# Kernel tuning notes

Hardware: AMD Instinct MI355X
Metric: run time of the kernel (lower is better)

The kernel has to match this reference:

```python
import jax, jax.numpy as jnp
import numpy as np
import math

B, T, D, H = 4, 1024, 512, 8
DH = D // H


def setup_inputs() -> dict:
    key = jax.random.key(0)
    ks = jax.random.split(key, 8)
    s = 1.0 / math.sqrt(D)
    return {
        "x": jax.random.normal(ks[0], (B, T, D), jnp.float32),
        "Wq_w": jax.random.normal(ks[1], (D, D), jnp.float32) * s,
        "Wq_b": jnp.zeros((D,), jnp.float32),
        "Wk_w": jax.random.normal(ks[2], (D, D), jnp.float32) * s,
        "Wk_b": jnp.zeros((D,), jnp.float32),
        "Wv_w": jax.random.normal(ks[3], (D, D), jnp.float32) * s,
        "Wv_b": jnp.zeros((D,), jnp.float32),
        "Ws_w": jax.random.normal(ks[4], (D, H), jnp.float32) * s,
        "Ws_b": jnp.zeros((H,), jnp.float32),
        "Wo_w": jax.random.normal(ks[5], (D, D), jnp.float32) * s,
        "Wo_b": jnp.zeros((D,), jnp.float32),
    }


def reference(x, Wq_w, Wq_b, Wk_w, Wk_b, Wv_w, Wv_b, Ws_w, Ws_b, Wo_w, Wo_b):
    b, t, d = x.shape
    # projections (weights stored [in, out]; same math as torch Linear)
    q = (x @ Wq_w + Wq_b).reshape(b, t, H, DH).transpose(0, 2, 1, 3)  # [B,H,T,dh]
    k = (x @ Wk_w + Wk_b).reshape(b, t, H, DH).transpose(0, 2, 1, 3)
    v = (x @ Wv_w + Wv_b).reshape(b, t, H, DH).transpose(0, 2, 1, 3)

    logits = jnp.einsum("bhtd,bhsd->bhts", q, k) / math.sqrt(DH)
    series = jax.nn.softmax(logits, axis=-1)  # [B,H,T,T] (dropout p=0 -> no-op)

    sigma = jax.nn.softplus(x @ Ws_w + Ws_b).transpose(0, 2, 1) + 1e-6  # [B,H,T]

    idx = jnp.arange(t, dtype=jnp.float32)
    dist2 = (idx[None, :] - idx[:, None]) ** 2  # [T,T]
    s2 = sigma[..., None] ** 2 + 1e-6           # [B,H,T,1]
    prior = jnp.exp(-dist2[None, None] / (2.0 * s2))
    prior = prior / (prior.sum(axis=-1, keepdims=True) + 1e-9)

    out = jnp.einsum("bhts,bhsd->bhtd", series, v)
    out = out.transpose(0, 2, 1, 3).reshape(b, t, d)
    out = out @ Wo_w + Wo_b
    return out, series, prior, sigma
```

## Files before the change

### kernel.cpp

```cpp
#include <hip/hip_runtime.h>
#include <math.h>

#define BB 4
#define TT 1024
#define DD 512
#define HH 8
#define DHH 64

typedef short bf8_t __attribute__((ext_vector_type(8)));
typedef float f32x4 __attribute__((ext_vector_type(4)));

__device__ __forceinline__ float softplus_f(float z) {
    return fmaxf(z, 0.f) + log1pf(__expf(-fabsf(z)));
}

__device__ __forceinline__ unsigned short f2bf(float f) {
    union { float f; unsigned int u; } v; v.f = f;
    return (unsigned short)((v.u + 0x7FFFu + ((v.u >> 16) & 1u)) >> 16);
}

__device__ __forceinline__ void bar_lgkm() {
    asm volatile("s_waitcnt lgkmcnt(0)" ::: "memory");
    __builtin_amdgcn_s_barrier();
}

__global__ __launch_bounds__(256) void cast_x_kernel(
    const float* __restrict__ x, unsigned short* __restrict__ xbf)
{
    int i = blockIdx.x * 256 + threadIdx.x;
    float4 a = *(const float4*)&x[(size_t)i * 8];
    float4 b = *(const float4*)&x[(size_t)i * 8 + 4];
    union { unsigned short u[8]; int4 v; } o;
    o.u[0] = f2bf(a.x); o.u[1] = f2bf(a.y); o.u[2] = f2bf(a.z); o.u[3] = f2bf(a.w);
    o.u[4] = f2bf(b.x); o.u[5] = f2bf(b.y); o.u[6] = f2bf(b.z); o.u[7] = f2bf(b.w);
    *(int4*)&xbf[(size_t)i * 8] = o.v;
}

__global__ __launch_bounds__(256) void transpose_w_kernel(
    const float* __restrict__ Wq, const float* __restrict__ Wk,
    const float* __restrict__ Wv, const float* __restrict__ Wo,
    const float* __restrict__ Ws,
    unsigned short* __restrict__ wt, unsigned short* __restrict__ woT)
{
    __shared__ float tile[32][33];
    const int tid = threadIdx.x;
    const int z = blockIdx.z;
    if (z == 4) {
        if (blockIdx.x != 0 || blockIdx.y != 0) return;
        #pragma unroll
        for (int i = 0; i < 16; ++i) {
            int idx = i * 256 + tid;
            int k = idx >> 3, n = idx & 7;
            wt[(size_t)(1536 + n) * 512 + k] = f2bf(Ws[idx]);
        }
        return;
    }
    const float* W = (z == 0) ? Wq : (z == 1) ? Wk : (z == 2) ? Wv : Wo;
    unsigned short* dst = (z < 3) ? (wt + (size_t)z * 512 * 512) : woT;
    const int k0 = blockIdx.x * 32, n0 = blockIdx.y * 32;
    const int ty = tid >> 3, tx = tid & 7;

    float4 v = *(const float4*)&W[(size_t)(k0 + ty) * 512 + n0 + tx * 4];
    tile[ty][tx*4+0] = v.x; tile[ty][tx*4+1] = v.y;
    tile[ty][tx*4+2] = v.z; tile[ty][tx*4+3] = v.w;
    __syncthreads();
    ushort4 o;
    o.x = f2bf(tile[tx*4+0][ty]);
    o.y = f2bf(tile[tx*4+1][ty]);
    o.z = f2bf(tile[tx*4+2][ty]);
    o.w = f2bf(tile[tx*4+3][ty]);
    *(ushort4*)&dst[(size_t)(n0 + ty) * 512 + k0 + tx * 4] = o;
}

__global__ __launch_bounds__(256) void proj_mfma_kernel(
    const unsigned short* __restrict__ xbf,
    const unsigned short* __restrict__ wt,
    const float* __restrict__ bq, const float* __restrict__ bk,
    const float* __restrict__ bv, const float* __restrict__ bs,
    unsigned short* __restrict__ qbf, unsigned short* __restrict__ kbf,
    unsigned short* __restrict__ vbf, float* __restrict__ sigma_out)
{
    __shared__ unsigned short a_s[64][64];
    __shared__ unsigned short b_s[64][64];
    const int tid = threadIdx.x;
    const int w = tid >> 6, l = tid & 63, lr = l & 15, lg = l >> 4;
    const int ct = blockIdx.x;
    const int m0 = blockIdx.y * 64;
    const int n0 = ct * 64;

    f32x4 acc[4];
    #pragma unroll
    for (int nb = 0; nb < 4; ++nb) acc[nb] = (f32x4){0.f, 0.f, 0.f, 0.f};

    for (int k0 = 0; k0 < 512; k0 += 64) {
        __syncthreads();
        #pragma unroll
        for (int rep = 0; rep < 2; ++rep) {
            int idx = rep * 256 + tid;
            int row = idx >> 3, cg = idx & 7;
            *(int4*)&a_s[row][(cg ^ (row & 7)) * 8] =
                *(const int4*)&xbf[(size_t)(m0 + row) * 512 + k0 + cg * 8];
            *(int4*)&b_s[row][(cg ^ (row & 7)) * 8] =
                *(const int4*)&wt[(size_t)(n0 + row) * 512 + k0 + cg * 8];
        }
        __syncthreads();
        #pragma unroll
        for (int ks = 0; ks < 2; ++ks) {
            int arow = w * 16 + lr;
            bf8_t af = *(const bf8_t*)&a_s[arow][((ks*4 + lg) ^ (arow & 7)) * 8];
            #pragma unroll
            for (int nb = 0; nb < 4; ++nb) {
                int brow = nb * 16 + lr;
                bf8_t bf = *(const bf8_t*)&b_s[brow][((ks*4 + lg) ^ (brow & 7)) * 8];
                acc[nb] = __builtin_amdgcn_mfma_f32_16x16x32_bf16(af, bf, acc[nb], 0, 0, 0);
            }
        }
    }

    if (ct < 24) {
        const int seg = ct >> 3;
        const int h = ct & 7;
        const float* bias = (seg == 0) ? bq : (seg == 1) ? bk : bv;
        unsigned short* dst = (seg == 0) ? qbf : (seg == 1) ? kbf : vbf;
        const float sc = (seg == 0) ? 0.125f : 1.f;
        #pragma unroll
        for (int nb = 0; nb < 4; ++nb) {
            float bb = bias[h * 64 + nb * 16 + lr];
            #pragma unroll
            for (int r = 0; r < 4; ++r) {
                int m = m0 + w * 16 + lg * 4 + r;
                int b = m >> 10, t = m & 1023;
                dst[((size_t)((b*HH + h)*TT + t)) * 64 + nb * 16 + lr] =
                    f2bf((acc[nb][r] + bb) * sc);
            }
        }
    } else if (lr < 8) {
        float bb = bs[lr];
        #pragma unroll
        for (int r = 0; r < 4; ++r) {
            int m = m0 + w * 16 + lg * 4 + r;
            int b = m >> 10, t = m & 1023;
            sigma_out[(size_t)(b*HH + lr)*TT + t] = softplus_f(acc[0][r] + bb) + 1e-6f;
        }
    }
}

__global__ __launch_bounds__(256) void attn_kernel(
    const unsigned short* __restrict__ qbf,
    const unsigned short* __restrict__ kbf,
    const unsigned short* __restrict__ vbf,
    const float* __restrict__ sigma,
    float* __restrict__ series, float* __restrict__ prior,
    unsigned short* __restrict__ obf)
{
    __shared__ unsigned short k_lds[2][64][72];
    __shared__ unsigned short v_lds[2][64][64];
    __shared__ unsigned short p_lds[4][16][72];

    const int tid = threadIdx.x;
    const int w  = tid >> 6, l = tid & 63;
    const int lr = l & 15,  lg = l >> 4;
    const int bh = blockIdx.y;
    const int qr = blockIdx.x * 64 + w * 16;

    const int srow = tid >> 3, scg = tid & 7;
    const unsigned short* kb = kbf + (size_t)bh * TT * 64;
    const unsigned short* vb = vbf + (size_t)bh * TT * 64;

    bf8_t aq[2];
    {
        const unsigned short* qrow = &qbf[((size_t)bh * TT + qr + lr) * 64];
        aq[0] = *(const bf8_t*)&qrow[lg * 8];
        aq[1] = *(const bf8_t*)&qrow[32 + lg * 8];
    }

    int4 kreg0, kreg1, vreg0, vreg1;

    float psum[4] = {0.f, 0.f, 0.f, 0.f};
    kreg0 = *(const int4*)&kb[(size_t)srow * 64 + scg * 8];
    kreg1 = *(const int4*)&kb[(size_t)(32 + srow) * 64 + scg * 8];
    *(int4*)&k_lds[0][srow][scg * 8] = kreg0;
    *(int4*)&k_lds[0][32 + srow][scg * 8] = kreg1;
    bar_lgkm();

    for (int st = 0; st < 16; ++st) {
        const int cur = st & 1;
        if (st < 15) {
            kreg0 = *(const int4*)&kb[(size_t)((st+1)*64 + srow) * 64 + scg * 8];
            kreg1 = *(const int4*)&kb[(size_t)((st+1)*64 + 32 + srow) * 64 + scg * 8];
        }
        #pragma unroll
        for (int nb = 0; nb < 4; ++nb) {
            f32x4 acc = {0.f, 0.f, 0.f, 0.f};
            #pragma unroll
            for (int c = 0; c < 2; ++c) {
                bf8_t bk = *(const bf8_t*)&k_lds[cur][nb * 16 + lr][c * 32 + lg * 8];
                acc = __builtin_amdgcn_mfma_f32_16x16x32_bf16(aq[c], bk, acc, 0, 0, 0);
            }
            #pragma unroll
            for (int r = 0; r < 4; ++r) psum[r] += __expf(acc[r]);
        }
        if (st < 15) {
            *(int4*)&k_lds[cur ^ 1][srow][scg * 8] = kreg0;
            *(int4*)&k_lds[cur ^ 1][32 + srow][scg * 8] = kreg1;
            bar_lgkm();
        }
    }
    #pragma unroll
    for (int r = 0; r < 4; ++r) {
        psum[r] += __shfl_xor(psum[r], 1);
        psum[r] += __shfl_xor(psum[r], 2);
        psum[r] += __shfl_xor(psum[r], 4);
        psum[r] += __shfl_xor(psum[r], 8);
    }
    float inv[4];
    #pragma unroll
    for (int r = 0; r < 4; ++r) inv[r] = 1.f / psum[r];

    f32x4 oacc[4];
    #pragma unroll
    for (int nb = 0; nb < 4; ++nb) oacc[nb] = (f32x4){0.f, 0.f, 0.f, 0.f};

    kreg0 = *(const int4*)&kb[(size_t)srow * 64 + scg * 8];
    kreg1 = *(const int4*)&kb[(size_t)(32 + srow) * 64 + scg * 8];
    vreg0 = *(const int4*)&vb[(size_t)srow * 64 + scg * 8];
    vreg1 = *(const int4*)&vb[(size_t)(32 + srow) * 64 + scg * 8];
    *(int4*)&k_lds[0][srow][scg * 8] = kreg0;
    *(int4*)&k_lds[0][32 + srow][scg * 8] = kreg1;
    {
        const unsigned short* pv0 = (const unsigned short*)&vreg0;
        const unsigned short* pv1 = (const unsigned short*)&vreg1;
        #pragma unroll
        for (int j = 0; j < 8; ++j) {
            int row = scg * 8 + j;
            int g0 = ((srow >> 3) ^ j ^ scg) & 7;
            int g1 = ((srow >> 3) ^ 4 ^ j ^ scg) & 7;
            v_lds[0][row][g0 * 8 + (srow & 7)] = pv0[j];
            v_lds[0][row][g1 * 8 + (srow & 7)] = pv1[j];
        }
    }
    bar_lgkm();

    for (int st = 0; st < 16; ++st) {
        const int cur = st & 1;
        if (st < 15) {
            kreg0 = *(const int4*)&kb[(size_t)((st+1)*64 + srow) * 64 + scg * 8];
            kreg1 = *(const int4*)&kb[(size_t)((st+1)*64 + 32 + srow) * 64 + scg * 8];
            vreg0 = *(const int4*)&vb[(size_t)((st+1)*64 + srow) * 64 + scg * 8];
            vreg1 = *(const int4*)&vb[(size_t)((st+1)*64 + 32 + srow) * 64 + scg * 8];
        }

        #pragma unroll
        for (int nb = 0; nb < 4; ++nb) {
            f32x4 acc = {0.f, 0.f, 0.f, 0.f};
            #pragma unroll
            for (int c = 0; c < 2; ++c) {
                bf8_t bk = *(const bf8_t*)&k_lds[cur][nb * 16 + lr][c * 32 + lg * 8];
                acc = __builtin_amdgcn_mfma_f32_16x16x32_bf16(aq[c], bk, acc, 0, 0, 0);
            }
            #pragma unroll
            for (int r = 0; r < 4; ++r) {
                float e = __expf(acc[r]);
                series[((size_t)bh * TT + qr + lg * 4 + r) * TT + st * 64 + nb * 16 + lr]
                    = e * inv[r];
                p_lds[w][lg * 4 + r][nb * 16 + lr] = f2bf(e);
            }
        }

        bf8_t pa0 = *(const bf8_t*)&p_lds[w][lr][lg * 8];
        bf8_t pa1 = *(const bf8_t*)&p_lds[w][lr][32 + lg * 8];
        #pragma unroll
        for (int nb = 0; nb < 4; ++nb) {
            #pragma unroll
            for (int c = 0; c < 2; ++c) {
                int row = nb * 16 + lr;
                int gsw = ((c * 4 + lg) ^ (row & 7) ^ (row >> 3)) & 7;
                bf8_t bv = *(const bf8_t*)&v_lds[cur][row][gsw * 8];
                oacc[nb] = __builtin_amdgcn_mfma_f32_16x16x32_bf16(
                    (c == 0) ? pa0 : pa1, bv, oacc[nb], 0, 0, 0);
            }
        }

        {
            int t = qr + st;
            float sg = sigma[(size_t)bh * TT + t];
            float cc = 1.f / (2.f * (sg * sg + 1e-6f));
            float e[16]; float sum = 0.f;
            #pragma unroll
            for (int j = 0; j < 16; ++j) {
                float d = (float)(t - (j * 64 + l));
                e[j] = __expf(-(d * d) * cc);
                sum += e[j];
            }
            sum += __shfl_xor(sum, 32);
            sum += __shfl_xor(sum, 16);
            sum += __shfl_xor(sum, 8);
            sum += __shfl_xor(sum, 4);
            sum += __shfl_xor(sum, 2);
            sum += __shfl_xor(sum, 1);
            float pinv = 1.f / (sum + 1e-9f);
            float* pr = prior + ((size_t)bh * TT + t) * TT;
            #pragma unroll
            for (int j = 0; j < 16; ++j) pr[j * 64 + l] = e[j] * pinv;
        }

        if (st < 15) {
            *(int4*)&k_lds[cur ^ 1][srow][scg * 8] = kreg0;
            *(int4*)&k_lds[cur ^ 1][32 + srow][scg * 8] = kreg1;
            const unsigned short* pv0 = (const unsigned short*)&vreg0;
            const unsigned short* pv1 = (const unsigned short*)&vreg1;
            #pragma unroll
            for (int j = 0; j < 8; ++j) {
                int row = scg * 8 + j;
                int g0 = ((srow >> 3) ^ j ^ scg) & 7;
                int g1 = ((srow >> 3) ^ 4 ^ j ^ scg) & 7;
                v_lds[cur ^ 1][row][g0 * 8 + (srow & 7)] = pv0[j];
                v_lds[cur ^ 1][row][g1 * 8 + (srow & 7)] = pv1[j];
            }
            bar_lgkm();
        }
    }

    const int b = bh >> 3, h = bh & 7;
    #pragma unroll
    for (int nb = 0; nb < 4; ++nb)
        #pragma unroll
        for (int r = 0; r < 4; ++r) {
            int t = qr + lg * 4 + r;
            obf[((size_t)(b * TT + t)) * 512 + h * 64 + nb * 16 + lr] =
                f2bf(oacc[nb][r] * inv[r]);
        }
}

__global__ __launch_bounds__(256) void outproj_mfma_kernel(
    const unsigned short* __restrict__ obf,
    const unsigned short* __restrict__ woT,
    const float* __restrict__ bo, float* __restrict__ out)
{
    __shared__ unsigned short a_s[64][64];
    __shared__ unsigned short b_s[64][64];
    const int tid = threadIdx.x;
    const int w = tid >> 6, l = tid & 63, lr = l & 15, lg = l >> 4;
    const int n0 = blockIdx.x * 64;
    const int m0 = blockIdx.y * 64;

    f32x4 acc[4];
    #pragma unroll
    for (int nb = 0; nb < 4; ++nb) acc[nb] = (f32x4){0.f, 0.f, 0.f, 0.f};

    for (int k0 = 0; k0 < 512; k0 += 64) {
        __syncthreads();
        #pragma unroll
        for (int rep = 0; rep < 2; ++rep) {
            int idx = rep * 256 + tid;
            int row = idx >> 3, cg = idx & 7;
            *(int4*)&a_s[row][(cg ^ (row & 7)) * 8] =
                *(const int4*)&obf[(size_t)(m0 + row) * 512 + k0 + cg * 8];
            *(int4*)&b_s[row][(cg ^ (row & 7)) * 8] =
                *(const int4*)&woT[(size_t)(n0 + row) * 512 + k0 + cg * 8];
        }
        __syncthreads();
        #pragma unroll
        for (int ks = 0; ks < 2; ++ks) {
            int arow = w * 16 + lr;
            bf8_t af = *(const bf8_t*)&a_s[arow][((ks*4 + lg) ^ (arow & 7)) * 8];
            #pragma unroll
            for (int nb = 0; nb < 4; ++nb) {
                int brow = nb * 16 + lr;
                bf8_t bf = *(const bf8_t*)&b_s[brow][((ks*4 + lg) ^ (brow & 7)) * 8];
                acc[nb] = __builtin_amdgcn_mfma_f32_16x16x32_bf16(af, bf, acc[nb], 0, 0, 0);
            }
        }
    }

    #pragma unroll
    for (int nb = 0; nb < 4; ++nb) {
        float bb = bo[n0 + nb * 16 + lr];
        #pragma unroll
        for (int r = 0; r < 4; ++r) {
            int m = m0 + w * 16 + lg * 4 + r;
            out[(size_t)m * 512 + n0 + nb * 16 + lr] = acc[nb][r] + bb;
        }
    }
}

extern "C" void kernel_launch(void* const* d_in, const int* in_sizes, int n_in,
                              void* d_out, int out_size, void* d_ws, size_t ws_size,
                              hipStream_t stream)
{
    const float* x    = (const float*)d_in[0];
    const float* Wq_w = (const float*)d_in[1];
    const float* Wq_b = (const float*)d_in[2];
    const float* Wk_w = (const float*)d_in[3];
    const float* Wk_b = (const float*)d_in[4];
    const float* Wv_w = (const float*)d_in[5];
    const float* Wv_b = (const float*)d_in[6];
    const float* Ws_w = (const float*)d_in[7];
    const float* Ws_b = (const float*)d_in[8];
    const float* Wo_w = (const float*)d_in[9];
    const float* Wo_b = (const float*)d_in[10];

    float* out    = (float*)d_out;
    float* series = out + (size_t)BB*TT*DD;
    float* prior  = series + (size_t)BB*HH*TT*TT;
    float* sigma  = prior + (size_t)BB*HH*TT*TT;

    const size_t nx = (size_t)BB*TT*DD;
    unsigned short* xbf = (unsigned short*)d_ws;
    unsigned short* wt  = xbf + nx;
    unsigned short* woT = wt + (size_t)1600*512;
    unsigned short* qbf = woT + (size_t)512*512;
    unsigned short* kbf = qbf + nx;
    unsigned short* vbf = kbf + nx;
    unsigned short* obf = vbf + nx;

    cast_x_kernel<<<1024, 256, 0, stream>>>(x, xbf);
    transpose_w_kernel<<<dim3(16, 16, 5), 256, 0, stream>>>(
        Wq_w, Wk_w, Wv_w, Wo_w, Ws_w, wt, woT);

    proj_mfma_kernel<<<dim3(25, 64), 256, 0, stream>>>(
        xbf, wt, Wq_b, Wk_b, Wv_b, Ws_b, qbf, kbf, vbf, sigma);

    attn_kernel<<<dim3(16, 32), 256, 0, stream>>>(
        qbf, kbf, vbf, sigma, series, prior, obf);

    outproj_mfma_kernel<<<dim3(8, 64), 256, 0, stream>>>(obf, woT, Wo_b, out);
}
```

Before: 105.4 us.

## Double-buffer GEMM LDS tiles with register prefetch and merge prep kernels

The projection and output-projection GEMMs now use two LDS buffers and prefetch the next K chunk into registers while MFMAs run on the current one, which halves the barriers per iteration. The cast and weight-transpose kernels are merged into one launch with a flat block index. This targets global-load latency in small GEMMs and the overhead of one extra kernel launch. In exchange it doubles LDS use and adds register pressure, which may lower occupancy.

After: 106.7 us. No clear change (+1.2%).

```diff
diff --git a/kernel.cpp b/kernel.cpp
--- a/kernel.cpp
+++ b/kernel.cpp
@@ -24,52 +24,53 @@
     __builtin_amdgcn_s_barrier();
 }
 
-__global__ __launch_bounds__(256) void cast_x_kernel(
-    const float* __restrict__ x, unsigned short* __restrict__ xbf)
-{
-    int i = blockIdx.x * 256 + threadIdx.x;
-    float4 a = *(const float4*)&x[(size_t)i * 8];
-    float4 b = *(const float4*)&x[(size_t)i * 8 + 4];
-    union { unsigned short u[8]; int4 v; } o;
-    o.u[0] = f2bf(a.x); o.u[1] = f2bf(a.y); o.u[2] = f2bf(a.z); o.u[3] = f2bf(a.w);
-    o.u[4] = f2bf(b.x); o.u[5] = f2bf(b.y); o.u[6] = f2bf(b.z); o.u[7] = f2bf(b.w);
-    *(int4*)&xbf[(size_t)i * 8] = o.v;
-}
-
-__global__ __launch_bounds__(256) void transpose_w_kernel(
+__global__ __launch_bounds__(256) void prep_kernel(
+    const float* __restrict__ x,
     const float* __restrict__ Wq, const float* __restrict__ Wk,
     const float* __restrict__ Wv, const float* __restrict__ Wo,
     const float* __restrict__ Ws,
+    unsigned short* __restrict__ xbf,
     unsigned short* __restrict__ wt, unsigned short* __restrict__ woT)
 {
     __shared__ float tile[32][33];
     const int tid = threadIdx.x;
-    const int z = blockIdx.z;
-    if (z == 4) {
-        if (blockIdx.x != 0 || blockIdx.y != 0) return;
-        #pragma unroll
-        for (int i = 0; i < 16; ++i) {
-            int idx = i * 256 + tid;
-            int k = idx >> 3, n = idx & 7;
-            wt[(size_t)(1536 + n) * 512 + k] = f2bf(Ws[idx]);
-        }
+    int b = blockIdx.x;
+
+    if (b < 1024) {
+        int i = b * 256 + tid;
+        float4 a = *(const float4*)&x[(size_t)i * 8];
+        float4 c = *(const float4*)&x[(size_t)i * 8 + 4];
+        union { unsigned short u[8]; int4 v; } o;
+        o.u[0] = f2bf(a.x); o.u[1] = f2bf(a.y); o.u[2] = f2bf(a.z); o.u[3] = f2bf(a.w);
+        o.u[4] = f2bf(c.x); o.u[5] = f2bf(c.y); o.u[6] = f2bf(c.z); o.u[7] = f2bf(c.w);
+        *(int4*)&xbf[(size_t)i * 8] = o.v;
         return;
     }
-    const float* W = (z == 0) ? Wq : (z == 1) ? Wk : (z == 2) ? Wv : Wo;
-    unsigned short* dst = (z < 3) ? (wt + (size_t)z * 512 * 512) : woT;
-    const int k0 = blockIdx.x * 32, n0 = blockIdx.y * 32;
-    const int ty = tid >> 3, tx = tid & 7;
-
-    float4 v = *(const float4*)&W[(size_t)(k0 + ty) * 512 + n0 + tx * 4];
-    tile[ty][tx*4+0] = v.x; tile[ty][tx*4+1] = v.y;
-    tile[ty][tx*4+2] = v.z; tile[ty][tx*4+3] = v.w;
-    __syncthreads();
-    ushort4 o;
-    o.x = f2bf(tile[tx*4+0][ty]);
-    o.y = f2bf(tile[tx*4+1][ty]);
-    o.z = f2bf(tile[tx*4+2][ty]);
-    o.w = f2bf(tile[tx*4+3][ty]);
-    *(ushort4*)&dst[(size_t)(n0 + ty) * 512 + k0 + tx * 4] = o;
+    b -= 1024;
+    if (b < 1024) {
+        int z = b >> 8, t = b & 255;
+        const float* W = (z == 0) ? Wq : (z == 1) ? Wk : (z == 2) ? Wv : Wo;
+        unsigned short* dst = (z < 3) ? (wt + (size_t)z * 512 * 512) : woT;
+        int k0 = (t >> 4) * 32, n0 = (t & 15) * 32;
+        int ty = tid >> 3, tx = tid & 7;
+        float4 v = *(const float4*)&W[(size_t)(k0 + ty) * 512 + n0 + tx * 4];
+        tile[ty][tx*4+0] = v.x; tile[ty][tx*4+1] = v.y;
+        tile[ty][tx*4+2] = v.z; tile[ty][tx*4+3] = v.w;
+        __syncthreads();
+        ushort4 o;
+        o.x = f2bf(tile[tx*4+0][ty]);
+        o.y = f2bf(tile[tx*4+1][ty]);
+        o.z = f2bf(tile[tx*4+2][ty]);
+        o.w = f2bf(tile[tx*4+3][ty]);
+        *(ushort4*)&dst[(size_t)(n0 + ty) * 512 + k0 + tx * 4] = o;
+        return;
+    }
+    #pragma unroll
+    for (int i = 0; i < 16; ++i) {
+        int idx = i * 256 + tid;
+        int k = idx >> 3, n = idx & 7;
+        wt[(size_t)(1536 + n) * 512 + k] = f2bf(Ws[idx]);
+    }
 }
 
 __global__ __launch_bounds__(256) void proj_mfma_kernel(
@@ -80,8 +81,8 @@
     unsigned short* __restrict__ qbf, unsigned short* __restrict__ kbf,
     unsigned short* __restrict__ vbf, float* __restrict__ sigma_out)
 {
-    __shared__ unsigned short a_s[64][64];
-    __shared__ unsigned short b_s[64][64];
+    __shared__ unsigned short a_s[2][64][64];
+    __shared__ unsigned short b_s[2][64][64];
     const int tid = threadIdx.x;
     const int w = tid >> 6, l = tid & 63, lr = l & 15, lg = l >> 4;
     const int ct = blockIdx.x;
@@ -92,28 +93,56 @@
     #pragma unroll
     for (int nb = 0; nb < 4; ++nb) acc[nb] = (f32x4){0.f, 0.f, 0.f, 0.f};
 
-    for (int k0 = 0; k0 < 512; k0 += 64) {
-        __syncthreads();
-        #pragma unroll
-        for (int rep = 0; rep < 2; ++rep) {
-            int idx = rep * 256 + tid;
-            int row = idx >> 3, cg = idx & 7;
-            *(int4*)&a_s[row][(cg ^ (row & 7)) * 8] =
-                *(const int4*)&xbf[(size_t)(m0 + row) * 512 + k0 + cg * 8];
-            *(int4*)&b_s[row][(cg ^ (row & 7)) * 8] =
-                *(const int4*)&wt[(size_t)(n0 + row) * 512 + k0 + cg * 8];
-        }
-        __syncthreads();
+    int4 areg[2], breg[2];
+
+    #pragma unroll
+    for (int rep = 0; rep < 2; ++rep) {
+        int idx = rep * 256 + tid;
+        int row = idx >> 3, cg = idx & 7;
+        areg[rep] = *(const int4*)&xbf[(size_t)(m0 + row) * 512 + cg * 8];
+        breg[rep] = *(const int4*)&wt[(size_t)(n0 + row) * 512 + cg * 8];
+    }
+    #pragma unroll
+    for (int rep = 0; rep < 2; ++rep) {
+        int idx = rep * 256 + tid;
+        int row = idx >> 3, cg = idx & 7;
+        *(int4*)&a_s[0][row][(cg ^ (row & 7)) * 8] = areg[rep];
+        *(int4*)&b_s[0][row][(cg ^ (row & 7)) * 8] = breg[rep];
+    }
+    bar_lgkm();
+
+    for (int kc = 0; kc < 8; ++kc) {
+        const int cur = kc & 1;
+        if (kc < 7) {
+            int k0 = (kc + 1) * 64;
+            #pragma unroll
+            for (int rep = 0; rep < 2; ++rep) {
+                int idx = rep * 256 + tid;
+                int row = idx >> 3, cg = idx & 7;
+                areg[rep] = *(const int4*)&xbf[(size_t)(m0 + row) * 512 + k0 + cg * 8];
+                breg[rep] = *(const int4*)&wt[(size_t)(n0 + row) * 512 + k0 + cg * 8];
+            }
+        }
         #pragma unroll
         for (int ks = 0; ks < 2; ++ks) {
             int arow = w * 16 + lr;
-            bf8_t af = *(const bf8_t*)&a_s[arow][((ks*4 + lg) ^ (arow & 7)) * 8];
+            bf8_t af = *(const bf8_t*)&a_s[cur][arow][((ks*4 + lg) ^ (arow & 7)) * 8];
             #pragma unroll
             for (int nb = 0; nb < 4; ++nb) {
                 int brow = nb * 16 + lr;
-                bf8_t bf = *(const bf8_t*)&b_s[brow][((ks*4 + lg) ^ (brow & 7)) * 8];
+                bf8_t bf = *(const bf8_t*)&b_s[cur][brow][((ks*4 + lg) ^ (brow & 7)) * 8];
                 acc[nb] = __builtin_amdgcn_mfma_f32_16x16x32_bf16(af, bf, acc[nb], 0, 0, 0);
             }
+        }
+        if (kc < 7) {
+            #pragma unroll
+            for (int rep = 0; rep < 2; ++rep) {
+                int idx = rep * 256 + tid;
+                int row = idx >> 3, cg = idx & 7;
+                *(int4*)&a_s[cur ^ 1][row][(cg ^ (row & 7)) * 8] = areg[rep];
+                *(int4*)&b_s[cur ^ 1][row][(cg ^ (row & 7)) * 8] = breg[rep];
+            }
+            bar_lgkm();
         }
     }
 
@@ -337,8 +366,8 @@
     const unsigned short* __restrict__ woT,
     const float* __restrict__ bo, float* __restrict__ out)
 {
-    __shared__ unsigned short a_s[64][64];
-    __shared__ unsigned short b_s[64][64];
+    __shared__ unsigned short a_s[2][64][64];
+    __shared__ unsigned short b_s[2][64][64];
     const int tid = threadIdx.x;
     const int w = tid >> 6, l = tid & 63, lr = l & 15, lg = l >> 4;
     const int n0 = blockIdx.x * 64;
@@ -348,28 +377,55 @@
     #pragma unroll
     for (int nb = 0; nb < 4; ++nb) acc[nb] = (f32x4){0.f, 0.f, 0.f, 0.f};
 
-    for (int k0 = 0; k0 < 512; k0 += 64) {
-        __syncthreads();
-        #pragma unroll
-        for (int rep = 0; rep < 2; ++rep) {
-            int idx = rep * 256 + tid;
-            int row = idx >> 3, cg = idx & 7;
-            *(int4*)&a_s[row][(cg ^ (row & 7)) * 8] =
-                *(const int4*)&obf[(size_t)(m0 + row) * 512 + k0 + cg * 8];
-            *(int4*)&b_s[row][(cg ^ (row & 7)) * 8] =
-                *(const int4*)&woT[(size_t)(n0 + row) * 512 + k0 + cg * 8];
-        }
-        __syncthreads();
+    int4 areg[2], breg[2];
+    #pragma unroll
+    for (int rep = 0; rep < 2; ++rep) {
+        int idx = rep * 256 + tid;
+        int row = idx >> 3, cg = idx & 7;
+        areg[rep] = *(const int4*)&obf[(size_t)(m0 + row) * 512 + cg * 8];
+        breg[rep] = *(const int4*)&woT[(size_t)(n0 + row) * 512 + cg * 8];
+    }
+    #pragma unroll
+    for (int rep = 0; rep < 2; ++rep) {
+        int idx = rep * 256 + tid;
+        int row = idx >> 3, cg = idx & 7;
+        *(int4*)&a_s[0][row][(cg ^ (row & 7)) * 8] = areg[rep];
+        *(int4*)&b_s[0][row][(cg ^ (row & 7)) * 8] = breg[rep];
+    }
+    bar_lgkm();
+
+    for (int kc = 0; kc < 8; ++kc) {
+        const int cur = kc & 1;
+        if (kc < 7) {
+            int k0 = (kc + 1) * 64;
+            #pragma unroll
+            for (int rep = 0; rep < 2; ++rep) {
+                int idx = rep * 256 + tid;
+                int row = idx >> 3, cg = idx & 7;
+                areg[rep] = *(const int4*)&obf[(size_t)(m0 + row) * 512 + k0 + cg * 8];
+                breg[rep] = *(const int4*)&woT[(size_t)(n0 + row) * 512 + k0 + cg * 8];
+            }
+        }
         #pragma unroll
         for (int ks = 0; ks < 2; ++ks) {
             int arow = w * 16 + lr;
-            bf8_t af = *(const bf8_t*)&a_s[arow][((ks*4 + lg) ^ (arow & 7)) * 8];
+            bf8_t af = *(const bf8_t*)&a_s[cur][arow][((ks*4 + lg) ^ (arow & 7)) * 8];
             #pragma unroll
             for (int nb = 0; nb < 4; ++nb) {
                 int brow = nb * 16 + lr;
-                bf8_t bf = *(const bf8_t*)&b_s[brow][((ks*4 + lg) ^ (brow & 7)) * 8];
+                bf8_t bf = *(const bf8_t*)&b_s[cur][brow][((ks*4 + lg) ^ (brow & 7)) * 8];
                 acc[nb] = __builtin_amdgcn_mfma_f32_16x16x32_bf16(af, bf, acc[nb], 0, 0, 0);
             }
+        }
+        if (kc < 7) {
+            #pragma unroll
+            for (int rep = 0; rep < 2; ++rep) {
+                int idx = rep * 256 + tid;
+                int row = idx >> 3, cg = idx & 7;
+                *(int4*)&a_s[cur ^ 1][row][(cg ^ (row & 7)) * 8] = areg[rep];
+                *(int4*)&b_s[cur ^ 1][row][(cg ^ (row & 7)) * 8] = breg[rep];
+            }
+            bar_lgkm();
         }
     }
 
@@ -414,9 +470,8 @@
     unsigned short* vbf = kbf + nx;
     unsigned short* obf = vbf + nx;
 
-    cast_x_kernel<<<1024, 256, 0, stream>>>(x, xbf);
-    transpose_w_kernel<<<dim3(16, 16, 5), 256, 0, stream>>>(
-        Wq_w, Wk_w, Wv_w, Wo_w, Ws_w, wt, woT);
+    prep_kernel<<<2049, 256, 0, stream>>>(
+        x, Wq_w, Wk_w, Wv_w, Wo_w, Ws_w, xbf, wt, woT);
 
     proj_mfma_kernel<<<dim3(25, 64), 256, 0, stream>>>(
         xbf, wt, Wq_b, Wk_b, Wv_b, Ws_b, qbf, kbf, vbf, sigma);
```
